# Kernel tuning notes

Measured on AMD Instinct MI355X. Metric: run time of the kernel, lower is better.

The kernel has to match this reference:

```python
import jax, jax.numpy as jnp
import numpy as np

EMBED_DIM = 1024
BATCH, SEQ = 4, 2048


def setup_inputs() -> dict:
    key = jax.random.key(0)
    kx, kq, kk, kv = jax.random.split(key, 4)
    return {
        "x": jax.random.normal(kx, (BATCH, SEQ, EMBED_DIM), dtype=jnp.float32),
        "q_weight": jax.random.normal(kq, (EMBED_DIM, EMBED_DIM), dtype=jnp.float32),
        "k_weight": jax.random.normal(kk, (EMBED_DIM, EMBED_DIM), dtype=jnp.float32),
        "v_weight": jax.random.normal(kv, (EMBED_DIM, EMBED_DIM), dtype=jnp.float32),
    }


def reference(x, q_weight, k_weight, v_weight):
    # x: [b, s, d]
    d = x.shape[-1]
    Q = jnp.einsum('bsd,de->bse', x, q_weight)
    K = jnp.einsum('bsd,de->bse', x, k_weight)
    V = jnp.einsum('bsd,de->bse', x, v_weight)
    scores = jnp.einsum('bqe,bke->bqk', Q, K) / jnp.sqrt(jnp.float32(d))
    attn = jax.nn.softmax(scores, axis=-1)
    out = jnp.einsum('bqk,bke->bqe', attn, V)
    return out
```

## Files before the change

kernel.cpp:

```cpp
#include <hip/hip_runtime.h>
#include <hip/hip_bf16.h>


typedef _Float16 half8 __attribute__((ext_vector_type(8)));
typedef _Float16 half4v __attribute__((ext_vector_type(4)));
typedef float f32x16 __attribute__((ext_vector_type(16)));

#define GLOBAL_AS __attribute__((address_space(1)))
#define LDS_AS __attribute__((address_space(3)))

__device__ __forceinline__ void gll16(const _Float16* g, _Float16* l) {
    __builtin_amdgcn_global_load_lds((GLOBAL_AS const void*)g, (LDS_AS void*)l, 16, 0, 0);
}

template <int NPROD, int OUTMODE>
__global__ __launch_bounds__(256) void gemm_nt(
    const _Float16* __restrict__ A0, const _Float16* __restrict__ A1,
    const _Float16* __restrict__ B0, const _Float16* __restrict__ B1,
    float* __restrict__ Cf, _Float16* __restrict__ C0, _Float16* __restrict__ C1,
    int lda, int ldb, int ldc, int K,
    long sA, long sB, long sC, float scale, float scale2) {
    constexpr int NTILES = (NPROD == 3) ? 4 : 2;
    constexpr int BUFH = NTILES * 4096;
    __shared__ alignas(16) _Float16 smem[2 * BUFH];

    const int tid = threadIdx.x;
    const int wave = tid >> 6, lane = tid & 63;
    const int wm = (wave >> 1) * 64, wn = (wave & 1) * 64;
    const int q2 = lane >> 5, r32 = lane & 31;

    const long zA = (long)blockIdx.z * sA;
    const long zB = (long)blockIdx.z * sB;
    const long zC = (long)blockIdx.z * sC;

    const float sc = (blockIdx.y * 2 < gridDim.y) ? scale : scale2;

    const int trow = tid >> 2;
    const int tcol = (((tid & 3) - ((tid >> 3) & 3) - ((tid >> 6) & 3)) & 3) * 8;
    const _Float16* gA0 = A0 + zA + (long)(blockIdx.x * 128 + trow) * lda + tcol;
    const _Float16* gB0 = B0 + zB + (long)(blockIdx.y * 128 + trow) * ldb + tcol;
    const _Float16* gA1 = (NPROD == 3) ? (A1 + zA + (long)(blockIdx.x * 128 + trow) * lda + tcol) : nullptr;
    const _Float16* gB1 = (NPROD == 3) ? (B1 + zB + (long)(blockIdx.y * 128 + trow) * ldb + tcol) : nullptr;

    f32x16 acc[2][2];
#pragma unroll
    for (int i = 0; i < 2; ++i)
#pragma unroll
        for (int j = 0; j < 2; ++j)
#pragma unroll
            for (int r = 0; r < 16; ++r) acc[i][j][r] = 0.f;

    const int ldsoff = tid * 8;
    const int fbase = q2 + (r32 >> 1) + (r32 >> 4);

    {
        _Float16* s = smem;
        gll16(gA0, s + ldsoff);
        gll16(gA0 + 64 * lda, s + ldsoff + 2048);
        gll16(gB0, s + 4096 + ldsoff);
        gll16(gB0 + 64 * ldb, s + 4096 + ldsoff + 2048);
        if (NPROD == 3) {
            gll16(gA1, s + 8192 + ldsoff);
            gll16(gA1 + 64 * lda, s + 8192 + ldsoff + 2048);
            gll16(gB1, s + 12288 + ldsoff);
            gll16(gB1 + 64 * ldb, s + 12288 + ldsoff + 2048);
        }
        gA0 += 32; gB0 += 32;
        if (NPROD == 3) { gA1 += 32; gB1 += 32; }
    }

    int buf = 0;
    for (int k0 = 0; k0 < K; k0 += 32) {
        __syncthreads();

        if (k0 + 32 < K) {
            _Float16* s = smem + (buf ^ 1) * BUFH;
            gll16(gA0, s + ldsoff);
            gll16(gA0 + 64 * lda, s + ldsoff + 2048);
            gll16(gB0, s + 4096 + ldsoff);
            gll16(gB0 + 64 * ldb, s + 4096 + ldsoff + 2048);
            if (NPROD == 3) {
                gll16(gA1, s + 8192 + ldsoff);
                gll16(gA1 + 64 * lda, s + 8192 + ldsoff + 2048);
                gll16(gB1, s + 12288 + ldsoff);
                gll16(gB1 + 64 * ldb, s + 12288 + ldsoff + 2048);
            }
            gA0 += 32; gB0 += 32;
            if (NPROD == 3) { gA1 += 32; gB1 += 32; }
        }

        _Float16* sA0 = smem + buf * BUFH;
        _Float16* sB0 = sA0 + 4096;
        _Float16* sA1 = (NPROD == 3) ? sA0 + 8192 : sA0;
        _Float16* sB1 = (NPROD == 3) ? sA0 + 12288 : sA0;
#pragma unroll
        for (int h = 0; h < 2; ++h) {
            half8 a0[2], b0[2], a1[2], b1[2];
#pragma unroll
            for (int i = 0; i < 2; ++i) {
                const int pp = ((fbase + 2 * i + 2 * h) & 3) * 8;
                a0[i] = *(const half8*)(sA0 + (wm + i * 32 + r32) * 32 + pp);
                b0[i] = *(const half8*)(sB0 + (wn + i * 32 + r32) * 32 + pp);
                if (NPROD == 3) {
                    a1[i] = *(const half8*)(sA1 + (wm + i * 32 + r32) * 32 + pp);
                    b1[i] = *(const half8*)(sB1 + (wn + i * 32 + r32) * 32 + pp);
                }
            }
#pragma unroll
            for (int i = 0; i < 2; ++i)
#pragma unroll
                for (int j = 0; j < 2; ++j) {
                    acc[i][j] = __builtin_amdgcn_mfma_f32_32x32x16_f16(a0[i], b0[j], acc[i][j], 0, 0, 0);
                    if (NPROD == 3) {
                        acc[i][j] = __builtin_amdgcn_mfma_f32_32x32x16_f16(a0[i], b1[j], acc[i][j], 0, 0, 0);
                        acc[i][j] = __builtin_amdgcn_mfma_f32_32x32x16_f16(a1[i], b0[j], acc[i][j], 0, 0, 0);
                    }
                }
        }
        buf ^= 1;
    }

    const int crow0 = blockIdx.x * 128 + wm + 4 * q2;
    const int ccol0 = blockIdx.y * 128 + wn + r32;
#pragma unroll
    for (int i = 0; i < 2; ++i)
#pragma unroll
        for (int j = 0; j < 2; ++j)
#pragma unroll
            for (int r = 0; r < 16; ++r) {
                int row = crow0 + i * 32 + (r & 3) + 8 * (r >> 2);
                long off = zC + (long)row * ldc + (ccol0 + j * 32);
                float v = acc[i][j][r] * sc;
                if (OUTMODE == 0) {
                    Cf[off] = v;
                } else if (OUTMODE == 2) {
                    C0[off] = (_Float16)v;
                } else {
                    _Float16 h = (_Float16)v;
                    C0[off] = h;
                    C1[off] = (_Float16)(v - (float)h);
                }
            }
}

__global__ __launch_bounds__(256) void prep_fused(
    const float* __restrict__ x, _Float16* __restrict__ x0, _Float16* __restrict__ x1,
    long n4, int nsplit,
    const float* __restrict__ wq, const float* __restrict__ wk,
    const float* __restrict__ wv,
    _Float16* __restrict__ qk0, _Float16* __restrict__ qk1,
    _Float16* __restrict__ v0, _Float16* __restrict__ v1) {
    __shared__ float t[32][33];
    if ((int)blockIdx.x < nsplit) {
        long i = (long)blockIdx.x * 256 + threadIdx.x;
        if (i >= n4) return;
        float4 v = ((const float4*)x)[i];
        float a[4] = {v.x, v.y, v.z, v.w};
        half4v h, l;
#pragma unroll
        for (int c = 0; c < 4; ++c) {
            h[c] = (_Float16)a[c];
            l[c] = (_Float16)(a[c] - (float)h[c]);
        }
        ((half4v*)x0)[i] = h;
        ((half4v*)x1)[i] = l;
        return;
    }
    const int idx = blockIdx.x - nsplit;
    const int z = idx >> 10;
    const int tile = idx & 1023;
    const float* in = (z == 0) ? wq : (z == 1) ? wk : wv;
    _Float16* o0 = (z == 0) ? qk0 : (z == 1) ? qk0 + 1024 * 1024 : v0;
    _Float16* o1 = (z == 0) ? qk1 : (z == 1) ? qk1 + 1024 * 1024 : v1;

    const int c0 = (tile & 31) * 32, r0 = (tile >> 5) * 32;
    const int tx = threadIdx.x & 31, ty = threadIdx.x >> 5;
#pragma unroll
    for (int i = 0; i < 32; i += 8)
        t[ty + i][tx] = in[(long)(r0 + ty + i) * 1024 + c0 + tx];
    __syncthreads();
#pragma unroll
    for (int i = 0; i < 32; i += 8) {
        float v = t[tx][ty + i];
        _Float16 h = (_Float16)v;
        long o = (long)(c0 + ty + i) * 1024 + r0 + tx;
        o0[o] = h;
        o1[o] = (_Float16)(v - (float)h);
    }
}

__global__ __launch_bounds__(256) void softmax_rows(const float* __restrict__ S,
                                                    _Float16* __restrict__ P) {
    const int n = 2048;
    const long base = (long)blockIdx.x * n;
    const float4* row4 = (const float4*)(S + base);
    const int tid = threadIdx.x;
    const int wave = tid >> 6;

    float4 v0 = row4[tid * 2];
    float4 v1 = row4[tid * 2 + 1];
    float v[8] = {v0.x, v0.y, v0.z, v0.w, v1.x, v1.y, v1.z, v1.w};
    float lm = -3.4e38f;
#pragma unroll
    for (int t = 0; t < 8; ++t) lm = fmaxf(lm, v[t]);
#pragma unroll
    for (int o = 32; o > 0; o >>= 1) lm = fmaxf(lm, __shfl_xor(lm, o));
    __shared__ float redm[4];
    __shared__ float reds[4];
    if ((tid & 63) == 0) redm[wave] = lm;
    __syncthreads();
    lm = fmaxf(fmaxf(redm[0], redm[1]), fmaxf(redm[2], redm[3]));

    float e[8];
    float ls = 0.f;
#pragma unroll
    for (int t = 0; t < 8; ++t) {
        e[t] = __expf(v[t] - lm);
        ls += e[t];
    }
#pragma unroll
    for (int o = 32; o > 0; o >>= 1) ls += __shfl_xor(ls, o);
    if ((tid & 63) == 0) reds[wave] = ls;
    __syncthreads();
    ls = reds[0] + reds[1] + reds[2] + reds[3];
    const float inv = 1.f / ls;
    half8 p;
#pragma unroll
    for (int t = 0; t < 8; ++t) p[t] = (_Float16)(e[t] * inv);
    ((half8*)(P + base))[tid] = p;
}

extern "C" void kernel_launch(void* const* d_in, const int* in_sizes, int n_in,
                              void* d_out, int out_size, void* d_ws, size_t ws_size,
                              hipStream_t stream) {
    (void)in_sizes; (void)n_in; (void)out_size; (void)ws_size;
    const float* x = (const float*)d_in[0];
    const float* wq = (const float*)d_in[1];
    const float* wk = (const float*)d_in[2];
    const float* wv = (const float*)d_in[3];
    float* out = (float*)d_out;
    char* ws = (char*)d_ws;

    const long MB = 1l << 20;
    _Float16* Wqk0 = (_Float16*)(ws + 0 * MB);
    _Float16* Wqk1 = (_Float16*)(ws + 4 * MB);
    _Float16* Wv0  = (_Float16*)(ws + 8 * MB);
    _Float16* Wv1  = (_Float16*)(ws + 10 * MB);
    _Float16* x0   = (_Float16*)(ws + 12 * MB);
    _Float16* x1   = (_Float16*)(ws + 28 * MB);
    _Float16* P    = (_Float16*)(ws + 12 * MB);
    _Float16* QK0  = (_Float16*)(ws + 44 * MB);
    _Float16* QK1  = (_Float16*)(ws + 76 * MB);
    _Float16* Vt   = (_Float16*)(ws + 108 * MB);
    float*    S    = (float*)(ws + 124 * MB);

    const int B = 4, SEQ = 2048, D = 1024;
    const long M = (long)B * SEQ;
    const long ssq = (long)SEQ * SEQ;
    const int nsplit = (int)((M * D / 4 + 255) / 256);

    prep_fused<<<dim3(nsplit + 3072), dim3(256), 0, stream>>>(
        x, x0, x1, M * D / 4, nsplit, wq, wk, wv, Wqk0, Wqk1, Wv0, Wv1);

    gemm_nt<3, 1><<<dim3(64, 16, 1), dim3(256), 0, stream>>>(
        x0, x1, Wqk0, Wqk1, nullptr, QK0, QK1, D, D, 2 * D, D,
        0, 0, 0, 0.03125f, 1.0f);

    gemm_nt<1, 2><<<dim3(8, 64, 1), dim3(256), 0, stream>>>(
        Wv0, nullptr, x0, nullptr, nullptr, Vt, nullptr, D, D, (int)M, D,
        0, 0, 0, 1.0f, 1.0f);

    gemm_nt<3, 0><<<dim3(16, 16, B), dim3(256), 0, stream>>>(
        QK0, QK1, QK0 + D, QK1 + D, S, nullptr, nullptr, 2 * D, 2 * D, SEQ, D,
        (long)SEQ * 2 * D, (long)SEQ * 2 * D, ssq, 1.0f, 1.0f);

    softmax_rows<<<dim3(B * SEQ), dim3(256), 0, stream>>>(S, P);

    gemm_nt<1, 0><<<dim3(16, 8, B), dim3(256), 0, stream>>>(
        P, nullptr, Vt, nullptr, out, nullptr, nullptr, SEQ, (int)M, D, SEQ,
        ssq, (long)SEQ, (long)SEQ * D, 1.0f, 1.0f);
}
```

Before: 394.9 us.

## Add 256x256 8-wave split-fp16 GEMM kernel for QK projection and scores

New measurement: 382.0 us. -3.3%, faster.

```diff
diff --git a/kernel.cpp b/kernel.cpp
--- a/kernel.cpp
+++ b/kernel.cpp
@@ -11,6 +11,18 @@
 
 __device__ __forceinline__ void gll16(const _Float16* g, _Float16* l) {
     __builtin_amdgcn_global_load_lds((GLOBAL_AS const void*)g, (LDS_AS void*)l, 16, 0, 0);
+}
+
+__device__ __forceinline__ void lgkm0_pin() {
+    asm volatile("s_waitcnt lgkmcnt(0)" ::: "memory");
+    __builtin_amdgcn_sched_barrier(0);
+}
+
+template <int N>
+__device__ __forceinline__ void vmwait() {
+    if constexpr (N == 0) asm volatile("s_waitcnt vmcnt(0)" ::: "memory");
+    else if constexpr (N == 4) asm volatile("s_waitcnt vmcnt(4)" ::: "memory");
+    else asm volatile("s_waitcnt vmcnt(8)" ::: "memory");
 }
 
 template <int NPROD, int OUTMODE>
@@ -143,6 +155,158 @@
             }
 }
 
+__device__ __forceinline__ void ld_a(half8 (&d)[4][2], const _Float16* base,
+                                     int wm, int r32, int fbase) {
+#pragma unroll
+    for (int i = 0; i < 4; ++i)
+#pragma unroll
+        for (int h = 0; h < 2; ++h)
+            d[i][h] = *(const half8*)(base + (wm + 32 * i + r32) * 32 +
+                                      ((fbase + 2 * i + 2 * h) & 3) * 8);
+}
+
+__device__ __forceinline__ void ld_b(half8 (&d)[2][2], const _Float16* base,
+                                     int wn, int r32, int fbase) {
+#pragma unroll
+    for (int j = 0; j < 2; ++j)
+#pragma unroll
+        for (int h = 0; h < 2; ++h)
+            d[j][h] = *(const half8*)(base + (wn + 32 * j + r32) * 32 +
+                                      ((fbase + 2 * j + 2 * h) & 3) * 8);
+}
+
+__device__ __forceinline__ void mfma_blk(f32x16 (&acc)[4][2], const half8 (&a)[4][2],
+                                         const half8 (&b)[2][2]) {
+#pragma unroll
+    for (int i = 0; i < 4; ++i)
+#pragma unroll
+        for (int j = 0; j < 2; ++j) {
+            acc[i][j] = __builtin_amdgcn_mfma_f32_32x32x16_f16(a[i][0], b[j][0], acc[i][j], 0, 0, 0);
+            acc[i][j] = __builtin_amdgcn_mfma_f32_32x32x16_f16(a[i][1], b[j][1], acc[i][j], 0, 0, 0);
+        }
+}
+
+__device__ __forceinline__ void stage_tile(_Float16* dst, const _Float16* g, int ld,
+                                           int ldsoff) {
+    gll16(g, dst + ldsoff);
+    gll16(g + (long)128 * ld, dst + 4096 + ldsoff);
+}
+
+template <int OUTMODE>
+__global__ __launch_bounds__(512, 2) void gemm8p(
+    const _Float16* __restrict__ A0, const _Float16* __restrict__ A1,
+    const _Float16* __restrict__ B0, const _Float16* __restrict__ B1,
+    float* __restrict__ Cf, _Float16* __restrict__ C0, _Float16* __restrict__ C1,
+    int lda, int ldb, int ldc, int K,
+    long sA, long sB, long sC, float scale, float scale2) {
+    __shared__ alignas(16) _Float16 smem[65536];
+
+    const int tid = threadIdx.x;
+    const int wave = tid >> 6, lane = tid & 63;
+    const int wm = (wave >> 2) * 128, wn = (wave & 3) * 64;
+    const int q2 = lane >> 5, r32 = lane & 31;
+
+    const long zA = (long)blockIdx.z * sA;
+    const long zB = (long)blockIdx.z * sB;
+    const long zC = (long)blockIdx.z * sC;
+    const float sc = (blockIdx.y * 2 < gridDim.y) ? scale : scale2;
+
+    const int trow = tid >> 2;
+    const int tcol = (((tid & 3) - ((tid >> 3) & 3) - ((tid >> 6) & 3)) & 3) * 8;
+    const _Float16* gA0 = A0 + zA + (long)(blockIdx.x * 256 + trow) * lda + tcol;
+    const _Float16* gB0 = B0 + zB + (long)(blockIdx.y * 256 + trow) * ldb + tcol;
+    const _Float16* gA1 = A1 + zA + (long)(blockIdx.x * 256 + trow) * lda + tcol;
+    const _Float16* gB1 = B1 + zB + (long)(blockIdx.y * 256 + trow) * ldb + tcol;
+
+    const int ldsoff = tid * 8;
+    const int fbase = q2 + (r32 >> 1) + (r32 >> 4);
+
+    f32x16 acc[4][2];
+#pragma unroll
+    for (int i = 0; i < 4; ++i)
+#pragma unroll
+        for (int j = 0; j < 2; ++j)
+#pragma unroll
+            for (int r = 0; r < 16; ++r) acc[i][j][r] = 0.f;
+
+    const int nT = K >> 5;
+
+    {
+        _Float16* s = smem;
+        stage_tile(s + 0, gA0, lda, ldsoff);
+        stage_tile(s + 8192, gB0, ldb, ldsoff);
+        stage_tile(s + 16384, gA1, lda, ldsoff);
+        stage_tile(s + 24576, gB1, ldb, ldsoff);
+        gA0 += 32; gB0 += 32; gA1 += 32; gB1 += 32;
+        vmwait<0>();
+        __builtin_amdgcn_s_barrier();
+    }
+
+    int buf = 0;
+    for (int t = 0; t < nT; ++t) {
+        _Float16* scur = smem + buf * 32768;
+        _Float16* snx = smem + (buf ^ 1) * 32768;
+        const bool pre = (t + 1 < nT);
+
+        half8 a0[4][2], b0[2][2], a1[4][2], b1[2][2];
+
+        ld_a(a0, scur, wm, r32, fbase);
+        ld_b(b0, scur + 8192, wn, r32, fbase);
+        if (pre) {
+            stage_tile(snx + 0, gA0, lda, ldsoff);
+            stage_tile(snx + 8192, gB0, ldb, ldsoff);
+            stage_tile(snx + 16384, gA1, lda, ldsoff);
+            stage_tile(snx + 24576, gB1, ldb, ldsoff);
+            gA0 += 32; gB0 += 32; gA1 += 32; gB1 += 32;
+        }
+        __builtin_amdgcn_s_barrier();
+        lgkm0_pin();
+        __builtin_amdgcn_s_setprio(1);
+        mfma_blk(acc, a0, b0);
+        __builtin_amdgcn_s_setprio(0);
+        __builtin_amdgcn_s_barrier();
+
+        ld_b(b1, scur + 24576, wn, r32, fbase);
+        __builtin_amdgcn_s_barrier();
+        lgkm0_pin();
+        __builtin_amdgcn_s_setprio(1);
+        mfma_blk(acc, a0, b1);
+        __builtin_amdgcn_s_setprio(0);
+        __builtin_amdgcn_s_barrier();
+
+        ld_a(a1, scur + 16384, wm, r32, fbase);
+        __builtin_amdgcn_s_barrier();
+        lgkm0_pin();
+        __builtin_amdgcn_s_setprio(1);
+        mfma_blk(acc, a1, b0);
+        __builtin_amdgcn_s_setprio(0);
+        if (pre) vmwait<0>();
+        __builtin_amdgcn_s_barrier();
+
+        buf ^= 1;
+    }
+
+    const int crow0 = blockIdx.x * 256 + wm + 4 * q2;
+    const int ccol0 = blockIdx.y * 256 + wn + r32;
+#pragma unroll
+    for (int i = 0; i < 4; ++i)
+#pragma unroll
+        for (int j = 0; j < 2; ++j)
+#pragma unroll
+            for (int r = 0; r < 16; ++r) {
+                int row = crow0 + i * 32 + (r & 3) + 8 * (r >> 2);
+                long off = zC + (long)row * ldc + (ccol0 + j * 32);
+                float v = acc[i][j][r] * sc;
+                if (OUTMODE == 0) {
+                    Cf[off] = v;
+                } else {
+                    _Float16 h = (_Float16)v;
+                    C0[off] = h;
+                    C1[off] = (_Float16)(v - (float)h);
+                }
+            }
+}
+
 __global__ __launch_bounds__(256) void prep_fused(
     const float* __restrict__ x, _Float16* __restrict__ x0, _Float16* __restrict__ x1,
     long n4, int nsplit,
@@ -262,7 +426,7 @@
     prep_fused<<<dim3(nsplit + 3072), dim3(256), 0, stream>>>(
         x, x0, x1, M * D / 4, nsplit, wq, wk, wv, Wqk0, Wqk1, Wv0, Wv1);
 
-    gemm_nt<3, 1><<<dim3(64, 16, 1), dim3(256), 0, stream>>>(
+    gemm8p<1><<<dim3(32, 8, 1), dim3(512), 0, stream>>>(
         x0, x1, Wqk0, Wqk1, nullptr, QK0, QK1, D, D, 2 * D, D,
         0, 0, 0, 0.03125f, 1.0f);
 
@@ -270,7 +434,7 @@
         Wv0, nullptr, x0, nullptr, nullptr, Vt, nullptr, D, D, (int)M, D,
         0, 0, 0, 1.0f, 1.0f);
 
-    gemm_nt<3, 0><<<dim3(16, 16, B), dim3(256), 0, stream>>>(
+    gemm8p<0><<<dim3(8, 8, B), dim3(512), 0, stream>>>(
         QK0, QK1, QK0 + D, QK1 + D, S, nullptr, nullptr, 2 * D, 2 * D, SEQ, D,
         (long)SEQ * 2 * D, (long)SEQ * 2 * D, ssq, 1.0f, 1.0f);
 
```
